# Optimization experiments

Hardware: AMD Instinct MI355X
Metric: run time of the kernel (lower is better)

Reference implementation:

```python
import jax, jax.numpy as jnp
import numpy as np

D_MODEL = 1024
NUM_HEADS = 16
BATCH = 2
SEQ = 2048


def setup_inputs() -> dict:
    key = jax.random.key(0)
    ks = jax.random.split(key, 5)
    scale = 1.0 / np.sqrt(D_MODEL)
    x = jax.random.normal(ks[0], (BATCH, SEQ, D_MODEL), dtype=jnp.float32)
    Wq = jax.random.normal(ks[1], (D_MODEL, D_MODEL), dtype=jnp.float32) * scale
    Wk = jax.random.normal(ks[2], (D_MODEL, D_MODEL), dtype=jnp.float32) * scale
    Wv = jax.random.normal(ks[3], (D_MODEL, D_MODEL), dtype=jnp.float32) * scale
    Wo = jax.random.normal(ks[4], (D_MODEL, D_MODEL), dtype=jnp.float32) * scale
    return {"x": x, "Wq": Wq, "Wk": Wk, "Wv": Wv, "Wo": Wo}


def reference(x, Wq, Wk, Wv, Wo):
    b, s, d_model = x.shape
    h = NUM_HEADS
    d_head = d_model // h
    # projections (Linear with weight [out,in]: y = x @ W^T)
    def split_heads(y):
        return y.reshape(b, s, h, d_head).transpose(0, 2, 1, 3)  # b h s d
    q = split_heads(x @ Wq.T)
    k = split_heads(x @ Wk.T)
    v = split_heads(x @ Wv.T)
    # full (non-flash) attention, as in the original
    att = jnp.einsum('bhsd,bhtd->bhst', q, k) / jnp.sqrt(jnp.float32(d_head)).astype(x.dtype)
    att = jax.nn.softmax(att, axis=-1)
    out = jnp.einsum('bhst,bhtd->bhsd', att, v)
    out = out.transpose(0, 2, 1, 3).reshape(b, s, d_model)
    return out @ Wo.T
```

## Files before the change

kernel.cpp:

```cpp
#include <hip/hip_runtime.h>
#include <stdint.h>

typedef __bf16 bf16_t;
typedef __bf16 bf16x4 __attribute__((ext_vector_type(4)));
typedef __bf16 bf16x8 __attribute__((ext_vector_type(8)));
typedef float  f32x4  __attribute__((ext_vector_type(4)));
typedef float  f32x16 __attribute__((ext_vector_type(16)));

#define D_MODEL 1024
#define SEQ     2048
#define BATCH   2
#define NHEAD   16
#define DHEAD   64
#define NROWS   (BATCH*SEQ)
#define LDT     72

__device__ __forceinline__ void async_ld16(const bf16_t* g, bf16_t* l) {
    __builtin_amdgcn_global_load_lds(
        (const __attribute__((address_space(1))) uint32_t*)(uintptr_t)g,
        (__attribute__((address_space(3))) uint32_t*)(uintptr_t)l,
        16, 0, 0);
}

__device__ __forceinline__ bf16x8 cvt8(f32x4 lo, f32x4 hi) {
    bf16x8 o;
#pragma unroll
    for (int i = 0; i < 4; ++i) { o[i] = (bf16_t)lo[i]; o[4 + i] = (bf16_t)hi[i]; }
    return o;
}

__device__ __forceinline__ bf16x4 shflx32(bf16x4 v) {
    union { bf16x4 b; long long u; } x;
    x.b = v;
    x.u = __shfl_xor(x.u, 32);
    return x.b;
}

__global__ void __launch_bounds__(256)
k_cvt(const float* __restrict__ w0, const float* __restrict__ w1,
      const float* __restrict__ w2, const float* __restrict__ w3,
      const float* __restrict__ x,
      bf16_t* __restrict__ o0, bf16_t* __restrict__ o1,
      bf16_t* __restrict__ o2, bf16_t* __restrict__ o3,
      bf16_t* __restrict__ ox)
{
    const int blk = blockIdx.x;
    const float* s; bf16_t* d; int bi;
    if (blk < 2048) { s = x; d = ox; bi = blk; }
    else {
        const int t = blk - 2048, sel = t >> 9; bi = t & 511;
        s = (sel == 0) ? w0 : (sel == 1) ? w1 : (sel == 2) ? w2 : w3;
        d = (sel == 0) ? o0 : (sel == 1) ? o1 : (sel == 2) ? o2 : o3;
    }
    const size_t i = ((size_t)bi * 256 + threadIdx.x) * 8;
    *(bf16x8*)(d + i) = cvt8(*(const f32x4*)(s + i), *(const f32x4*)(s + i + 4));
}

template <int OUT_MODE>
__device__ __forceinline__ void gemm128(bf16_t* __restrict__ smem,
                                        const bf16_t* __restrict__ X,
                                        const bf16_t* __restrict__ W,
                                        void* __restrict__ Yv,
                                        int m0, int n0, float oscale)
{
    bf16_t* lA = smem;
    bf16_t* lB = smem + 128 * 32;

    const int tid  = threadIdx.x;
    const int lane = tid & 63;
    const int w    = tid >> 6;
    const int l15  = lane & 15;
    const int quad = lane >> 4;

    const int c0 = tid, c1 = tid + 256;
    const int r0 = c0 >> 2, r1 = c1 >> 2;
    const int kc0 = (c0 & 3) ^ ((r0 >> 1) & 3);
    const int kc1 = (c1 & 3) ^ ((r1 >> 1) & 3);
    const bf16_t* gA0 = X + (size_t)(m0 + r0) * D_MODEL + kc0 * 8;
    const bf16_t* gA1 = X + (size_t)(m0 + r1) * D_MODEL + kc1 * 8;
    const bf16_t* gB0 = W + (size_t)(n0 + r0) * D_MODEL + kc0 * 8;
    const bf16_t* gB1 = W + (size_t)(n0 + r1) * D_MODEL + kc1 * 8;

    int am[4], bn[4];
    const int mw = (w >> 1) * 64, nw = (w & 1) * 64;
#pragma unroll
    for (int i = 0; i < 4; ++i) {
        const int ra = mw + i * 16 + l15;
        am[i] = ra * 32 + (quad ^ ((ra >> 1) & 3)) * 8;
        const int rb = nw + i * 16 + l15;
        bn[i] = rb * 32 + (quad ^ ((rb >> 1) & 3)) * 8;
    }

    f32x4 acc[4][4];
#pragma unroll
    for (int i = 0; i < 4; ++i)
#pragma unroll
        for (int j = 0; j < 4; ++j) acc[i][j] = f32x4{0.f, 0.f, 0.f, 0.f};

    for (int k0 = 0; k0 < D_MODEL; k0 += 32) {
        __syncthreads();
        async_ld16(gA0 + k0, &lA[c0 * 8]);
        async_ld16(gA1 + k0, &lA[c1 * 8]);
        async_ld16(gB0 + k0, &lB[c0 * 8]);
        async_ld16(gB1 + k0, &lB[c1 * 8]);
        __syncthreads();

        bf16x8 af[4], bfr[4];
#pragma unroll
        for (int i = 0; i < 4; ++i) af[i]  = *(const bf16x8*)&lA[am[i]];
#pragma unroll
        for (int i = 0; i < 4; ++i) bfr[i] = *(const bf16x8*)&lB[bn[i]];
#pragma unroll
        for (int mi = 0; mi < 4; ++mi)
#pragma unroll
            for (int ni = 0; ni < 4; ++ni)
                acc[mi][ni] = __builtin_amdgcn_mfma_f32_16x16x32_bf16(
                    af[mi], bfr[ni], acc[mi][ni], 0, 0, 0);
    }

    if constexpr (OUT_MODE == 1) {
        bf16_t* lT = smem;
#pragma unroll
        for (int h0 = 0; h0 < 2; ++h0) {
            __syncthreads();
            if ((w >> 1) == h0) {
#pragma unroll
                for (int mi = 0; mi < 4; ++mi)
#pragma unroll
                    for (int ni = 0; ni < 4; ++ni) {
                        bf16x4 pk;
#pragma unroll
                        for (int r = 0; r < 4; ++r)
                            pk[r] = (bf16_t)(acc[mi][ni][r] * oscale);
                        const int col = nw + ni * 16 + l15;
                        *(bf16x4*)&lT[col * LDT + mi * 16 + quad * 4] = pk;
                    }
            }
            __syncthreads();
            const int col = tid & 127;
            const int seg = tid >> 7;
            const int brow = m0 + h0 * 64;
            const int b = brow >> 11, sb = brow & 2047;
            const int cg = n0 + col;
            bf16_t* dst = (bf16_t*)Yv +
                ((size_t)((b << 4) | (cg >> 6)) * 64 + (cg & 63)) * SEQ + sb;
#pragma unroll
            for (int u = 0; u < 4; ++u)
                *(bf16x8*)(dst + seg * 32 + u * 8) =
                    *(const bf16x8*)&lT[col * LDT + seg * 32 + u * 8];
        }
    } else {
#pragma unroll
        for (int mi = 0; mi < 4; ++mi)
#pragma unroll
            for (int ni = 0; ni < 4; ++ni)
#pragma unroll
                for (int r = 0; r < 4; ++r) {
                    const int row = m0 + mw + mi * 16 + quad * 4 + r;
                    const int col = n0 + nw + ni * 16 + l15;
                    const float vv = acc[mi][ni][r] * oscale;
                    if constexpr (OUT_MODE == 0)
                        ((bf16_t*)Yv)[(size_t)row * D_MODEL + col] = (bf16_t)vv;
                    else
                        ((float*)Yv)[(size_t)row * D_MODEL + col] = vv;
                }
    }
}

__global__ void __launch_bounds__(256, 3)
k_gemm_qkv(const bf16_t* __restrict__ X,
           const bf16_t* __restrict__ Wq, const bf16_t* __restrict__ Wk,
           const bf16_t* __restrict__ Wv,
           bf16_t* __restrict__ Qb, bf16_t* __restrict__ Kb, bf16_t* __restrict__ Vt)
{
    __shared__ __align__(16) bf16_t smem[128 * LDT];
    const int sel = blockIdx.y >> 3;
    const int n0  = (blockIdx.y & 7) * 128;
    const int m0  = blockIdx.x * 128;
    if (sel == 0)      gemm128<0>(smem, X, Wq, Qb, m0, n0, 0.125f);
    else if (sel == 1) gemm128<0>(smem, X, Wk, Kb, m0, n0, 1.0f);
    else               gemm128<1>(smem, X, Wv, Vt, m0, n0, 1.0f);
}

__global__ void __launch_bounds__(256, 3)
k_gemm_out(const bf16_t* __restrict__ X, const bf16_t* __restrict__ W,
           float* __restrict__ Y)
{
    __shared__ __align__(16) bf16_t smem[128 * LDT];
    gemm128<2>(smem, X, W, Y, blockIdx.x * 128, blockIdx.y * 128, 1.0f);
}

__global__ void __launch_bounds__(256, 2)
k_attn(const bf16_t* __restrict__ Qb, const bf16_t* __restrict__ Kb,
       const bf16_t* __restrict__ Vt, bf16_t* __restrict__ Ob)
{
    __shared__ __align__(16) bf16_t lK[64 * 64];
    __shared__ __align__(16) bf16_t lV[64 * 64];
    __shared__ float sbuf[128];

    const int tid  = threadIdx.x;
    const int lane = tid & 63;
    const int w    = tid >> 6;
    const int l31  = lane & 31;
    const int h    = lane >> 5;

    const int bh = blockIdx.x;
    const int b_ = bh >> 4, hh = bh & 15;
    const int q0 = blockIdx.y * 128;

    const size_t base = (size_t)b_ * SEQ * D_MODEL + (size_t)hh * DHEAD;
    const bf16_t* Qp = Qb + base;
    const bf16_t* Kp = Kb + base;
    const bf16_t* Vp = Vt + (size_t)bh * DHEAD * SEQ;

    const int qrow = q0 + w * 32 + l31;
    bf16x8 qf[4];
#pragma unroll
    for (int c = 0; c < 4; ++c)
        qf[c] = *(const bf16x8*)&Qp[(size_t)qrow * D_MODEL + c * 16 + h * 8];

    const int c0 = tid, c1 = tid + 256;
    const int r0 = c0 >> 3, g0 = (c0 & 7) ^ (r0 & 7);
    const int r1 = r0 + 32;
    const bf16_t* gK0 = Kp + (size_t)r0 * D_MODEL + g0 * 8;
    const bf16_t* gK1 = Kp + (size_t)r1 * D_MODEL + g0 * 8;
    const bf16_t* gV0 = Vp + (size_t)r0 * SEQ + g0 * 8;
    const bf16_t* gV1 = Vp + (size_t)r1 * SEQ + g0 * 8;

    int koff[2][4], voff[2][4];
#pragma unroll
    for (int half = 0; half < 2; ++half)
#pragma unroll
        for (int c = 0; c < 4; ++c) {
            const int row = half * 32 + l31;
            koff[half][c] = row * 64 + ((2 * c + h) ^ (row & 7)) * 8;
            voff[half][c] = koff[half][c];
        }

    f32x16 acc_o[2];
#pragma unroll
    for (int a = 0; a < 2; ++a)
#pragma unroll
        for (int i = 0; i < 16; ++i) acc_o[a][i] = 0.f;
    float rsum = 0.f;

    for (int kv0 = 0; kv0 < SEQ; kv0 += 64) {
        __syncthreads();
        async_ld16(gK0 + (size_t)kv0 * D_MODEL, &lK[c0 * 8]);
        async_ld16(gK1 + (size_t)kv0 * D_MODEL, &lK[c1 * 8]);
        async_ld16(gV0 + kv0, &lV[c0 * 8]);
        async_ld16(gV1 + kv0, &lV[c1 * 8]);
        __syncthreads();

        bf16x4 pk[2][4];
#pragma unroll
        for (int half = 0; half < 2; ++half) {
            f32x16 st;
#pragma unroll
            for (int i = 0; i < 16; ++i) st[i] = 0.f;
#pragma unroll
            for (int c = 0; c < 4; ++c) {
                bf16x8 kf = *(const bf16x8*)&lK[koff[half][c]];
                st = __builtin_amdgcn_mfma_f32_32x32x16_bf16(kf, qf[c], st, 0, 0, 0);
            }
#pragma unroll
            for (int g = 0; g < 4; ++g)
#pragma unroll
                for (int r = 0; r < 4; ++r) {
                    const float e = __expf(st[g * 4 + r]);
                    rsum += e;
                    pk[half][g][r] = (bf16_t)e;
                }
        }

        bf16x4 pt[2][4];
#pragma unroll
        for (int half = 0; half < 2; ++half)
#pragma unroll
            for (int g = 0; g < 4; ++g) pt[half][g] = shflx32(pk[half][g]);

        bf16x8 pf[4];
#pragma unroll
        for (int c = 0; c < 4; ++c) {
            const int half = c >> 1, e = 2 * (c & 1);
            bf16x4 lo = h ? pt[half][e + 1] : pk[half][e];
            bf16x4 hi = h ? pk[half][e + 1] : pt[half][e];
#pragma unroll
            for (int i = 0; i < 4; ++i) { pf[c][i] = lo[i]; pf[c][4 + i] = hi[i]; }
        }

#pragma unroll
        for (int a = 0; a < 2; ++a)
#pragma unroll
            for (int c = 0; c < 4; ++c) {
                bf16x8 vf = *(const bf16x8*)&lV[voff[a][c]];
                acc_o[a] = __builtin_amdgcn_mfma_f32_32x32x16_bf16(
                    pf[c], vf, acc_o[a], 0, 0, 0);
            }
    }

    rsum += __shfl_xor(rsum, 32);
    if (h == 0) sbuf[w * 32 + l31] = rsum;
    __syncthreads();

#pragma unroll
    for (int a = 0; a < 2; ++a)
#pragma unroll
        for (int g = 0; g < 4; ++g)
#pragma unroll
            for (int r = 0; r < 4; ++r) {
                const int ql  = w * 32 + r + 8 * g + 4 * h;
                const int row = b_ * SEQ + q0 + ql;
                const int col = hh * DHEAD + a * 32 + l31;
                Ob[(size_t)row * D_MODEL + col] =
                    (bf16_t)(acc_o[a][g * 4 + r] / sbuf[ql]);
            }
}

extern "C" void kernel_launch(void* const* d_in, const int* in_sizes, int n_in,
                              void* d_out, int out_size, void* d_ws, size_t ws_size,
                              hipStream_t stream)
{
    const float* x  = (const float*)d_in[0];
    const float* Wq = (const float*)d_in[1];
    const float* Wk = (const float*)d_in[2];
    const float* Wv = (const float*)d_in[3];
    const float* Wo = (const float*)d_in[4];
    float* out = (float*)d_out;

    const size_t wmat = (size_t)D_MODEL * D_MODEL;
    const size_t mat  = (size_t)NROWS * D_MODEL;
    bf16_t* Wqb = (bf16_t*)d_ws;
    bf16_t* Wkb = Wqb + wmat;
    bf16_t* Wvb = Wkb + wmat;
    bf16_t* Wob = Wvb + wmat;
    bf16_t* Xb  = Wob + wmat;
    bf16_t* Qb  = Xb + mat;
    bf16_t* Kb  = Qb + mat;
    bf16_t* Vt  = Kb + mat;
    bf16_t* Ab  = Qb;

    dim3 blk(256);
    k_cvt<<<dim3(4096), blk, 0, stream>>>(Wq, Wk, Wv, Wo, x, Wqb, Wkb, Wvb, Wob, Xb);
    k_gemm_qkv<<<dim3(32, 24), blk, 0, stream>>>(Xb, Wqb, Wkb, Wvb, Qb, Kb, Vt);
    k_attn<<<dim3(32, 16), blk, 0, stream>>>(Qb, Kb, Vt, Ab);
    k_gemm_out<<<dim3(32, 8), blk, 0, stream>>>(Ab, Wob, out);
}
```

Before: 181.8 us.

## Double-buffer K/V tiles in attention and compute row sums via MFMA

The attention kernel now double-buffers the K and V tiles in LDS, prefetching the next tile asynchronously while computing on the current one, with one barrier per iteration instead of two. The softmax scale folds log2(e) into the Q projection so the kernel can use the native exp2. Row sums come from an extra MFMA against a ones vector rather than scalar adds and a shared-memory reduction. s_setprio hints are placed around the MFMA blocks. Doubling the LDS footprint may lower occupancy, and row sums are now taken over bf16-rounded probabilities.

```diff
diff --git a/kernel.cpp b/kernel.cpp
--- a/kernel.cpp
+++ b/kernel.cpp
@@ -14,6 +14,8 @@
 #define DHEAD   64
 #define NROWS   (BATCH*SEQ)
 #define LDT     72
+
+#define QSCALE  (0.125f * 1.4426950408889634f)
 
 __device__ __forceinline__ void async_ld16(const bf16_t* g, bf16_t* l) {
     __builtin_amdgcn_global_load_lds(
@@ -177,7 +179,7 @@
     const int sel = blockIdx.y >> 3;
     const int n0  = (blockIdx.y & 7) * 128;
     const int m0  = blockIdx.x * 128;
-    if (sel == 0)      gemm128<0>(smem, X, Wq, Qb, m0, n0, 0.125f);
+    if (sel == 0)      gemm128<0>(smem, X, Wq, Qb, m0, n0, QSCALE);
     else if (sel == 1) gemm128<0>(smem, X, Wk, Kb, m0, n0, 1.0f);
     else               gemm128<1>(smem, X, Wv, Vt, m0, n0, 1.0f);
 }
@@ -194,9 +196,8 @@
 k_attn(const bf16_t* __restrict__ Qb, const bf16_t* __restrict__ Kb,
        const bf16_t* __restrict__ Vt, bf16_t* __restrict__ Ob)
 {
-    __shared__ __align__(16) bf16_t lK[64 * 64];
-    __shared__ __align__(16) bf16_t lV[64 * 64];
-    __shared__ float sbuf[128];
+    __shared__ __align__(16) bf16_t lK[2][64 * 64];
+    __shared__ __align__(16) bf16_t lV[2][64 * 64];
 
     const int tid  = threadIdx.x;
     const int lane = tid & 63;
@@ -227,30 +228,42 @@
     const bf16_t* gV0 = Vp + (size_t)r0 * SEQ + g0 * 8;
     const bf16_t* gV1 = Vp + (size_t)r1 * SEQ + g0 * 8;
 
-    int koff[2][4], voff[2][4];
+    int koff[2][4];
 #pragma unroll
     for (int half = 0; half < 2; ++half)
 #pragma unroll
         for (int c = 0; c < 4; ++c) {
             const int row = half * 32 + l31;
             koff[half][c] = row * 64 + ((2 * c + h) ^ (row & 7)) * 8;
-            voff[half][c] = koff[half][c];
-        }
+        }
+
+    bf16x8 onef;
+#pragma unroll
+    for (int i = 0; i < 8; ++i) onef[i] = (bf16_t)1.0f;
 
     f32x16 acc_o[2];
-#pragma unroll
-    for (int a = 0; a < 2; ++a)
-#pragma unroll
-        for (int i = 0; i < 16; ++i) acc_o[a][i] = 0.f;
-    float rsum = 0.f;
-
-    for (int kv0 = 0; kv0 < SEQ; kv0 += 64) {
-        __syncthreads();
-        async_ld16(gK0 + (size_t)kv0 * D_MODEL, &lK[c0 * 8]);
-        async_ld16(gK1 + (size_t)kv0 * D_MODEL, &lK[c1 * 8]);
-        async_ld16(gV0 + kv0, &lV[c0 * 8]);
-        async_ld16(gV1 + kv0, &lV[c1 * 8]);
-        __syncthreads();
+    f32x16 acc_s;
+#pragma unroll
+    for (int i = 0; i < 16; ++i) { acc_o[0][i] = 0.f; acc_o[1][i] = 0.f; acc_s[i] = 0.f; }
+
+    async_ld16(gK0, &lK[0][c0 * 8]);
+    async_ld16(gK1, &lK[0][c1 * 8]);
+    async_ld16(gV0, &lV[0][c0 * 8]);
+    async_ld16(gV1, &lV[0][c1 * 8]);
+    asm volatile("s_waitcnt vmcnt(0)\n\ts_barrier" ::: "memory");
+
+    int cur = 0;
+    const int NT = SEQ / 64;
+    for (int t = 0; t < NT; ++t) {
+        if (t + 1 < NT) {
+            const int kv0 = (t + 1) * 64;
+            async_ld16(gK0 + (size_t)kv0 * D_MODEL, &lK[cur ^ 1][c0 * 8]);
+            async_ld16(gK1 + (size_t)kv0 * D_MODEL, &lK[cur ^ 1][c1 * 8]);
+            async_ld16(gV0 + kv0, &lV[cur ^ 1][c0 * 8]);
+            async_ld16(gV1 + kv0, &lV[cur ^ 1][c1 * 8]);
+        }
+        const bf16_t* lKc = lK[cur];
+        const bf16_t* lVc = lV[cur];
 
         bf16x4 pk[2][4];
 #pragma unroll
@@ -258,19 +271,18 @@
             f32x16 st;
 #pragma unroll
             for (int i = 0; i < 16; ++i) st[i] = 0.f;
+            __builtin_amdgcn_s_setprio(1);
 #pragma unroll
             for (int c = 0; c < 4; ++c) {
-                bf16x8 kf = *(const bf16x8*)&lK[koff[half][c]];
+                bf16x8 kf = *(const bf16x8*)&lKc[koff[half][c]];
                 st = __builtin_amdgcn_mfma_f32_32x32x16_bf16(kf, qf[c], st, 0, 0, 0);
             }
+            __builtin_amdgcn_s_setprio(0);
 #pragma unroll
             for (int g = 0; g < 4; ++g)
 #pragma unroll
-                for (int r = 0; r < 4; ++r) {
-                    const float e = __expf(st[g * 4 + r]);
-                    rsum += e;
-                    pk[half][g][r] = (bf16_t)e;
-                }
+                for (int r = 0; r < 4; ++r)
+                    pk[half][g][r] = (bf16_t)__builtin_amdgcn_exp2f(st[g * 4 + r]);
         }
 
         bf16x4 pt[2][4];
@@ -289,32 +301,35 @@
             for (int i = 0; i < 4; ++i) { pf[c][i] = lo[i]; pf[c][4 + i] = hi[i]; }
         }
 
+        __builtin_amdgcn_s_setprio(1);
+#pragma unroll
+        for (int c = 0; c < 4; ++c)
+            acc_s = __builtin_amdgcn_mfma_f32_32x32x16_bf16(pf[c], onef, acc_s, 0, 0, 0);
 #pragma unroll
         for (int a = 0; a < 2; ++a)
 #pragma unroll
             for (int c = 0; c < 4; ++c) {
-                bf16x8 vf = *(const bf16x8*)&lV[voff[a][c]];
+                bf16x8 vf = *(const bf16x8*)&lVc[koff[a][c]];
                 acc_o[a] = __builtin_amdgcn_mfma_f32_32x32x16_bf16(
                     pf[c], vf, acc_o[a], 0, 0, 0);
             }
-    }
-
-    rsum += __shfl_xor(rsum, 32);
-    if (h == 0) sbuf[w * 32 + l31] = rsum;
-    __syncthreads();
-
-#pragma unroll
-    for (int a = 0; a < 2; ++a)
-#pragma unroll
-        for (int g = 0; g < 4; ++g)
-#pragma unroll
-            for (int r = 0; r < 4; ++r) {
-                const int ql  = w * 32 + r + 8 * g + 4 * h;
-                const int row = b_ * SEQ + q0 + ql;
-                const int col = hh * DHEAD + a * 32 + l31;
-                Ob[(size_t)row * D_MODEL + col] =
-                    (bf16_t)(acc_o[a][g * 4 + r] / sbuf[ql]);
-            }
+        __builtin_amdgcn_s_setprio(0);
+
+        asm volatile("s_waitcnt vmcnt(0)\n\ts_barrier" ::: "memory");
+        cur ^= 1;
+    }
+
+#pragma unroll
+    for (int g = 0; g < 4; ++g)
+#pragma unroll
+        for (int r = 0; r < 4; ++r) {
+            const float inv = 1.0f / acc_s[g * 4 + r];
+            const int ql  = w * 32 + r + 8 * g + 4 * h;
+            const size_t rb = (size_t)(b_ * SEQ + q0 + ql) * D_MODEL
+                            + hh * DHEAD + l31;
+            Ob[rb]      = (bf16_t)(acc_o[0][g * 4 + r] * inv);
+            Ob[rb + 32] = (bf16_t)(acc_o[1][g * 4 + r] * inv);
+        }
 }
 
 extern "C" void kernel_launch(void* const* d_in, const int* in_sizes, int n_in,
```

Result: no change. 181.9 us (+0.1%).
